# Kernel optimization log

Hardware: AMD Instinct MI355X
Metric: run time of the kernel (lower is better)

## Reference

```python
import jax, jax.numpy as jnp
import numpy as np

N, E, L, F, HID, OUT = 20000, 200000, 5, 4, 128, 3


def _lin(x, w, b):
    # torch Linear convention: w is [out, in]
    return x @ w.T + b


def setup_inputs() -> dict:
    key = jax.random.key(0)
    ks = iter(jax.random.split(key, 40))
    nrm = lambda shape, s=0.05: jax.random.normal(next(ks), shape, dtype=jnp.float32) * s
    inp = {
        'x': jax.random.normal(next(ks), (N, L, F), dtype=jnp.float32),
        'edge_index': jax.random.randint(next(ks), (2, E), 0, N, dtype=jnp.int64),
        'edge_attr': jax.random.normal(next(ks), (E, F), dtype=jnp.float32),
        'batch': jnp.zeros((N,), dtype=jnp.int64),
        'node_type': jax.random.normal(next(ks), (N, 1), dtype=jnp.float32),
        # PastStateEncoder params
        'emb': nrm((L, F), 1.0),
        'conv_w': nrm((HID, 2 * F, 3)),  # Conv1d(8,128,3) OIW
        'conv_b': nrm((HID,)),
        # FusionLayer Linear(129,128)
        'fuse_w': nrm((HID, HID + 1)), 'fuse_b': nrm((HID,)),
        # gnn1 EdgeModel: Linear(2*128+4,128), Linear(128,128)
        'g1e_w1': nrm((HID, 2 * HID + F)), 'g1e_b1': nrm((HID,)),
        'g1e_w2': nrm((HID, HID)), 'g1e_b2': nrm((HID,)),
        # gnn1 NodeModel: Linear(256,128), Linear(128,128)
        'g1n_w1': nrm((HID, 2 * HID)), 'g1n_b1': nrm((HID,)),
        'g1n_w2': nrm((HID, HID)), 'g1n_b2': nrm((HID,)),
        # gnn2 EdgeModel: Linear(2*128+128,128), Linear(128,128)
        'g2e_w1': nrm((HID, 3 * HID)), 'g2e_b1': nrm((HID,)),
        'g2e_w2': nrm((HID, HID)), 'g2e_b2': nrm((HID,)),
        # gnn2 NodeModel
        'g2n_w1': nrm((HID, 2 * HID)), 'g2n_b1': nrm((HID,)),
        'g2n_w2': nrm((HID, HID)), 'g2n_b2': nrm((HID,)),
        # final_mlp: Linear(128,128), BN(128), Linear(128,3)
        'fm_w1': nrm((HID, HID)), 'fm_b1': nrm((HID,)),
        'bn_g': jnp.ones((HID,), dtype=jnp.float32), 'bn_b': jnp.zeros((HID,), dtype=jnp.float32),
        'fm_w2': nrm((OUT, HID)), 'fm_b2': nrm((OUT,)),
    }
    return inp


def _encoder(x, emb, conv_w, conv_b):
    # x: [N, L, F]; append learned positional embedding -> [N, L, 2F]
    n = x.shape[0]
    xe = jnp.concatenate([x, jnp.broadcast_to(emb[None], (n, L, F))], axis=-1)
    xc = xe.transpose(0, 2, 1)  # [N, 2F, L]
    y = jax.lax.conv_general_dilated(
        xc, conv_w, window_strides=(1,), padding=[(1, 1)],
        dimension_numbers=('NCW', 'OIW', 'NCW'))
    y = y + conv_b[None, :, None]
    return y.mean(axis=-1)  # [N, HID]


def _edge_mlp(src, dst, ea, w1, b1, w2, b2):
    h = jax.nn.relu(_lin(jnp.concatenate([src, dst, ea], axis=1), w1, b1))
    return _lin(h, w2, b2)


def _node_mlp(x_row, ea, w1, b1, w2, b2):
    h = jax.nn.relu(_lin(jnp.concatenate([x_row, ea], axis=1), w1, b1))
    return _lin(h, w2, b2)


def reference(x, edge_index, edge_attr, batch, node_type,
              emb, conv_w, conv_b, fuse_w, fuse_b,
              g1e_w1, g1e_b1, g1e_w2, g1e_b2, g1n_w1, g1n_b1, g1n_w2, g1n_b2,
              g2e_w1, g2e_b1, g2e_w2, g2e_b2, g2n_w1, g2n_b1, g2n_w2, g2n_b2,
              fm_w1, fm_b1, bn_g, bn_b, fm_w2, fm_b2):
    row, col = edge_index[0], edge_index[1]
    h = _encoder(x, emb, conv_w, conv_b)                     # [N,128]
    h = _lin(jnp.concatenate([h, node_type], axis=-1), fuse_w, fuse_b)  # [N,128]
    # gnn1 (MetaLayer: edge model then node model; node model here is per-edge)
    ea = _edge_mlp(h[row], h[col], edge_attr, g1e_w1, g1e_b1, g1e_w2, g1e_b2)  # [E,128]
    h = _node_mlp(h[row], ea, g1n_w1, g1n_b1, g1n_w2, g1n_b2)                  # [E,128]
    # gnn2 (h now lives on edges; indices < N <= E remain valid, matching torch)
    ea = _edge_mlp(h[row], h[col], ea, g2e_w1, g2e_b1, g2e_w2, g2e_b2)
    h = _node_mlp(h[row], ea, g2n_w1, g2n_b1, g2n_w2, g2n_b2)
    # final head on edge_attr: Linear -> BatchNorm1d (training stats) -> ReLU -> Linear
    z = _lin(ea, fm_w1, fm_b1)
    mu = z.mean(axis=0)
    var = z.var(axis=0)  # biased, matches torch BN normalization
    z = (z - mu) * jax.lax.rsqrt(var + 1e-5) * bn_g + bn_b
    z = jax.nn.relu(z)
    return _lin(z, fm_w2, fm_b2)  # [E,3]
```

## Files before the change

kernel.cpp:

```cpp
#include <hip/hip_runtime.h>

#define N_NODES 20000
#define N_EDGES 200000
#define HID 128
#define STR 136
#define NBLK 3125
#define NREP 64

typedef unsigned short u16;
using bf16x8 = __attribute__((ext_vector_type(8))) __bf16;
using f32x4  = __attribute__((ext_vector_type(4))) float;

__device__ __forceinline__ u16 f2bf(float f) {
  union { float f; unsigned u; } v; v.f = f;
  unsigned u = v.u;
  return (u16)((u + 0x7FFFu + ((u >> 16) & 1u)) >> 16);
}
__device__ __forceinline__ float bf2f(unsigned s) {
  union { unsigned u; float f; } v; v.u = s << 16;
  return v.f;
}
__device__ __forceinline__ bf16x8 ld8(const u16* p) { return *(const bf16x8*)p; }

__device__ __forceinline__ void zero_acc8(f32x4 acc[4]) {
#pragma unroll
  for (int i = 0; i < 4; ++i) acc[i] = (f32x4){0.f, 0.f, 0.f, 0.f};
}

template <int KSTEPS, typename AF>
__device__ __forceinline__ void wgemm8(const u16* __restrict__ PW, AF afrag,
                                       f32x4 acc[4], int lane, int wave) {
  const u16* pb = PW + (wave * 64 + lane) * 8;
  bf16x8 b[2];
  b[0] = ld8(pb);
#pragma unroll
  for (int ks = 0; ks < KSTEPS; ++ks) {
    const int cur = ks & 1;
    if (ks + 1 < KSTEPS) b[cur ^ 1] = ld8(pb + (ks + 1) * 4096);
#pragma unroll
    for (int mt = 0; mt < 4; ++mt) {
      bf16x8 a = afrag(ks, mt);
      acc[mt] = __builtin_amdgcn_mfma_f32_16x16x32_bf16(a, b[cur], acc[mt], 0, 0, 0);
    }
  }
}

template <bool RELU>
__device__ __forceinline__ void epi_store8(u16* buf, const f32x4 acc[4],
                                           const float* __restrict__ bias,
                                           int lane, int wave) {
  const int c = lane & 15, q = lane >> 4;
  const float bb = bias[wave * 16 + c];
  const int col = wave * 16 + c;
#pragma unroll
  for (int mt = 0; mt < 4; ++mt)
#pragma unroll
    for (int r = 0; r < 4; ++r) {
      float v = acc[mt][r] + bb;
      if (RELU) v = fmaxf(v, 0.f);
      buf[(mt * 16 + q * 4 + r) * STR + col] = f2bf(v);
    }
}

__device__ __forceinline__ void flush_buf8(const u16* buf, u16* __restrict__ gout,
                                           int e0, int tid) {
#pragma unroll
  for (int it = 0; it < 2; ++it) {
    int cid = tid + it * 512, e = cid >> 4, p = cid & 15;
    uint4 v = *(const uint4*)(buf + e * STR + p * 8);
    *(uint4*)(gout + (size_t)(e0 + e) * HID + p * 8) = v;
  }
}

__device__ __forceinline__ void stage_gather8(const int* __restrict__ rowI,
                                              const int* __restrict__ colI,
                                              const u16* __restrict__ htab,
                                              u16* B0, u16* B1,
                                              int e0, int lane, int wave) {
  const int r = lane >> 4, p = lane & 15;
#pragma unroll
  for (int it = 0; it < 4; ++it) {
    int j = wave * 16 + it * 4 + r;
    int e = j & 63;
    int id = (j < 64) ? rowI[e0 + e] : colI[e0 + e];
    uint4 v = *(const uint4*)(htab + (size_t)id * HID + p * 8);
    *(uint4*)(((j < 64) ? B0 : B1) + e * STR + p * 8) = v;
  }
}

__global__ __launch_bounds__(128) void k_prep1(
    const float* __restrict__ emb, const float* __restrict__ conv_w,
    const float* __restrict__ conv_b, const float* __restrict__ fuse_w,
    const float* __restrict__ fuse_b,
    const float* __restrict__ fm_w1, const float* __restrict__ g2e_b2,
    const float* __restrict__ fm_b1, const float* __restrict__ w6,
    float* __restrict__ Mt, float* __restrict__ C0, float* __restrict__ Wnt,
    float* __restrict__ b67, float* __restrict__ W67, float* __restrict__ bnrep) {
  __shared__ float red[22][129];
  __shared__ float w7s[128];
  const int o = blockIdx.x;
  const int j = threadIdx.x;
  bnrep[o * 128 + j] = 0.f;
  float A[21];
  {
    float b0 = conv_b[j];
#pragma unroll
    for (int p = 0; p < 5; ++p) {
#pragma unroll
      for (int i = 0; i < 8; ++i) {
        float s = 0.f;
#pragma unroll
        for (int k = 0; k < 3; ++k) {
          int t = p + 1 - k;
          if (t >= 0 && t < 5) s += conv_w[(j * 8 + i) * 3 + k];
        }
        s *= 0.2f;
        if (i < 4) A[p * 4 + i] = s;
        else b0 += emb[p * 4 + (i - 4)] * s;
      }
    }
    A[20] = b0;
  }
  float w = fuse_w[o * 129 + j];
  float w7 = fm_w1[o * 128 + j];
  w7s[j] = w7;
#pragma unroll
  for (int qq = 0; qq < 21; ++qq) red[qq][j] = w * A[qq];
  red[21][j] = w7 * g2e_b2[j];
  __syncthreads();
  if (j < 22) {
    float s = 0.f;
    for (int t = 0; t < 128; ++t) s += red[j][t];
    if (j < 20)      Mt[j * 128 + o] = s;
    else if (j == 20) C0[o] = s + fuse_b[o];
    else              b67[o] = s + fm_b1[o];
  }
  if (j == 0) Wnt[o] = fuse_w[o * 129 + 128];
  float s = 0.f;
  for (int t = 0; t < 128; ++t) s += w7s[t] * w6[t * 128 + j];
  W67[o * 128 + j] = s;
}

struct PackArgs {
  const float* src[6];
  u16* dst[6];
  int Kin[6];
  int ksCum[7];
};

__global__ __launch_bounds__(256) void k_prep2(
    PackArgs pa, const float* __restrict__ x, const float* __restrict__ node_type,
    const float* __restrict__ Mt, const float* __restrict__ C0,
    const float* __restrict__ Wnt, u16* __restrict__ h2) {
  if (blockIdx.x < 41) {
    int bk = blockIdx.x;
    int mi = 0;
    while (bk >= pa.ksCum[mi + 1]) ++mi;
    int ks = bk - pa.ksCum[mi];
    const float* W = pa.src[mi];
    u16* D = pa.dst[mi] + ks * 4096;
    int Kin = pa.Kin[mi];
#pragma unroll
    for (int t = 0; t < 16; ++t) {
      int el = t * 256 + (int)threadIdx.x;
      int j = el & 7, ln = (el >> 3) & 63, ntile = el >> 9;
      int k = ks * 32 + ((ln >> 4) << 3) + j;
      int n = ntile * 16 + (ln & 15);
      float v = (k < Kin) ? W[n * Kin + k] : 0.0f;
      D[el] = f2bf(v);
    }
    return;
  }
  __shared__ float xs[16][20], nts[16], mts[20 * 128];
  const int tid = threadIdx.x;
  const int n0 = ((int)blockIdx.x - 41) * 16;
  for (int i = tid; i < 320; i += 256) xs[i / 20][i % 20] = x[n0 * 20 + i];
  if (tid < 16) nts[tid] = node_type[n0 + tid];
  for (int i = tid; i < 2560; i += 256) mts[i] = Mt[i];
  __syncthreads();
  const int nl = tid >> 4;
  const int c0 = (tid & 15) * 8;
  float nt = nts[nl];
  union { u16 s[8]; uint4 u; } o;
#pragma unroll
  for (int i = 0; i < 8; ++i) {
    int ch = c0 + i;
    float acc = C0[ch] + Wnt[ch] * nt;
#pragma unroll
    for (int qq = 0; qq < 20; ++qq) acc += xs[nl][qq] * mts[qq * 128 + ch];
    o.s[i] = f2bf(acc);
  }
  *(uint4*)(h2 + (size_t)(n0 + nl) * HID + c0) = o.u;
}

__global__ __launch_bounds__(512, 8) void k_gnn1(
    const int* __restrict__ eidx, const float* __restrict__ eattr,
    const u16* __restrict__ h2, const u16* __restrict__ pW1, const u16* __restrict__ pW2,
    const u16* __restrict__ pW3, const u16* __restrict__ pW4, const float* __restrict__ b1,
    const float* __restrict__ b2, const float* __restrict__ b3, const float* __restrict__ b4,
    u16* __restrict__ ea1, u16* __restrict__ h3) {
  __shared__ __align__(16) u16 B0[64 * STR], B1[64 * STR];
  const int tid = threadIdx.x, lane = tid & 63, wave = tid >> 6;
  const int e0 = blockIdx.x * 64;
  const int m = lane & 15, q = lane >> 4;
  const int aoff = m * STR + q * 8;
  const int* rowI = eidx;
  const int* colI = eidx + N_EDGES;

  stage_gather8(rowI, colI, h2, B0, B1, e0, lane, wave);

  bf16x8 ef[4];
#pragma unroll
  for (int mt = 0; mt < 4; ++mt) {
    union { u16 s[8]; uint4 u; bf16x8 v; } t;
    t.u = make_uint4(0u, 0u, 0u, 0u);
    if (q == 0) {
      float4 a = *(const float4*)(eattr + (size_t)(e0 + mt * 16 + m) * 4);
      t.s[0] = f2bf(a.x); t.s[1] = f2bf(a.y); t.s[2] = f2bf(a.z); t.s[3] = f2bf(a.w);
    }
    ef[mt] = t.v;
  }
  __syncthreads();

  f32x4 acc[4];
  zero_acc8(acc);
  wgemm8<9>(pW1, [&](int ks, int mt) -> bf16x8 {
    if (ks < 4) return ld8(B0 + aoff + mt * 16 * STR + ks * 32);
    if (ks < 8) return ld8(B1 + aoff + mt * 16 * STR + (ks - 4) * 32);
    return ef[mt];
  }, acc, lane, wave);
  __syncthreads();
  epi_store8<true>(B1, acc, b1, lane, wave);
  __syncthreads();

  zero_acc8(acc);
  wgemm8<4>(pW2, [&](int ks, int mt) -> bf16x8 {
    return ld8(B1 + aoff + mt * 16 * STR + ks * 32);
  }, acc, lane, wave);
  epi_store8<false>(B0, acc, b2, lane, wave);
  __syncthreads();
  flush_buf8(B0, ea1, e0, tid);

  if (e0 < N_NODES) {
#pragma unroll
    for (int it = 0; it < 2; ++it) {
      int e = wave * 8 + it * 4 + q;
      int id = rowI[e0 + e];
      uint4 v = *(const uint4*)(h2 + (size_t)id * HID + m * 8);
      *(uint4*)(B1 + e * STR + m * 8) = v;
    }
    __syncthreads();

    zero_acc8(acc);
    wgemm8<8>(pW3, [&](int ks, int mt) -> bf16x8 {
      if (ks < 4) return ld8(B1 + aoff + mt * 16 * STR + ks * 32);
      return ld8(B0 + aoff + mt * 16 * STR + (ks - 4) * 32);
    }, acc, lane, wave);
    __syncthreads();
    epi_store8<true>(B1, acc, b3, lane, wave);
    __syncthreads();

    zero_acc8(acc);
    wgemm8<4>(pW4, [&](int ks, int mt) -> bf16x8 {
      return ld8(B1 + aoff + mt * 16 * STR + ks * 32);
    }, acc, lane, wave);
    epi_store8<false>(B0, acc, b4, lane, wave);
    __syncthreads();
    flush_buf8(B0, h3, e0, tid);
  }
}

__global__ __launch_bounds__(512, 8) void k_gnn2(
    const int* __restrict__ eidx, const u16* __restrict__ h3, u16* ea1z,
    const u16* __restrict__ pW5, const u16* __restrict__ pW67,
    const float* __restrict__ b5, const float* __restrict__ b67,
    float* __restrict__ bnrep) {
  __shared__ __align__(16) u16 B0[64 * STR], B1[64 * STR];
  const int tid = threadIdx.x, lane = tid & 63, wave = tid >> 6;
  const int e0 = blockIdx.x * 64;
  const int m = lane & 15, q = lane >> 4;
  const int aoff = m * STR + q * 8;
  const int* rowI = eidx;
  const int* colI = eidx + N_EDGES;

  stage_gather8(rowI, colI, h3, B0, B1, e0, lane, wave);
  __syncthreads();

  f32x4 acc[4];
  zero_acc8(acc);
  wgemm8<8>(pW5, [&](int ks, int mt) -> bf16x8 {
    if (ks < 4) return ld8(B0 + aoff + mt * 16 * STR + ks * 32);
    return ld8(B1 + aoff + mt * 16 * STR + (ks - 4) * 32);
  }, acc, lane, wave);
  __syncthreads();

#pragma unroll
  for (int it = 0; it < 2; ++it) {
    int cid = tid + it * 512, e = cid >> 4, p = cid & 15;
    uint4 v = *(const uint4*)(ea1z + (size_t)(e0 + e) * HID + p * 8);
    *(uint4*)(B0 + e * STR + p * 8) = v;
  }
  __syncthreads();

  wgemm8<4>(pW5 + 8 * 4096, [&](int ks, int mt) -> bf16x8 {
    return ld8(B0 + aoff + mt * 16 * STR + ks * 32);
  }, acc, lane, wave);
  epi_store8<true>(B1, acc, b5, lane, wave);
  __syncthreads();

  zero_acc8(acc);
  wgemm8<4>(pW67, [&](int ks, int mt) -> bf16x8 {
    return ld8(B1 + aoff + mt * 16 * STR + ks * 32);
  }, acc, lane, wave);

  {
    const int c = lane & 15;
    const int col = wave * 16 + c;
    const float bb = b67[col];
    float s0 = 0.f, q0 = 0.f;
#pragma unroll
    for (int mt = 0; mt < 4; ++mt)
#pragma unroll
      for (int r = 0; r < 4; ++r) {
        float v0 = acc[mt][r] + bb;
        s0 += v0; q0 += v0 * v0;
        int row = mt * 16 + q * 4 + r;
        B0[row * STR + col] = f2bf(v0);
      }
    s0 += __shfl_xor(s0, 16); s0 += __shfl_xor(s0, 32);
    q0 += __shfl_xor(q0, 16); q0 += __shfl_xor(q0, 32);
    if (lane < 16) {
      float* slot = bnrep + ((int)blockIdx.x & (NREP - 1)) * 256;
      atomicAdd(&slot[wave * 16 + lane], s0);
      atomicAdd(&slot[128 + wave * 16 + lane], q0);
    }
  }
  __syncthreads();
  flush_buf8(B0, ea1z, e0, tid);
}

__global__ __launch_bounds__(256) void k_head(const u16* __restrict__ z,
                                              const float* __restrict__ bnrep,
                                              const float* __restrict__ bn_g,
                                              const float* __restrict__ bn_b,
                                              const float* __restrict__ w2,
                                              const float* __restrict__ b2,
                                              float* __restrict__ out) {
  __shared__ float sh_s[128], sh_h[128], sh_w0[128], sh_w1[128], sh_w2[128];
  const int tid = threadIdx.x;
  {
    float s = 0.f;
    for (int r = 0; r < NREP; ++r) s += bnrep[r * 256 + tid];
    __shared__ float acc2[256];
    acc2[tid] = s;
    __syncthreads();
    if (tid < 128) {
      const float inv = 1.0f / (float)N_EDGES;
      float mu = acc2[tid] * inv;
      float var = acc2[128 + tid] * inv - mu * mu;
      float sc = bn_g[tid] * rsqrtf(var + 1e-5f);
      sh_s[tid] = sc;
      sh_h[tid] = bn_b[tid] - mu * sc;
      sh_w0[tid] = w2[tid];
      sh_w1[tid] = w2[128 + tid];
      sh_w2[tid] = w2[256 + tid];
    }
    __syncthreads();
  }
  const int lane = tid & 63, wave = tid >> 6;
  const int g = lane >> 4;
  const int p = lane & 15;
  const int c0 = p * 8;
  const float bb0 = b2[0], bb1 = b2[1], bb2 = b2[2];
#pragma unroll 4
  for (int it = 0; it < 16; ++it) {
    int e = (int)blockIdx.x * 256 + wave * 64 + it * 4 + g;
    if (e >= N_EDGES) break;
    uint4 v = *(const uint4*)(z + (size_t)e * HID + c0);
    unsigned wv[4] = {v.x, v.y, v.z, v.w};
    float a0 = 0.f, a1 = 0.f, a2 = 0.f;
#pragma unroll
    for (int k = 0; k < 4; ++k) {
      int ch = c0 + k * 2;
      float lo = bf2f(wv[k] & 0xffffu), hi = bf2f(wv[k] >> 16);
      float r0 = fmaxf(fmaf(lo, sh_s[ch], sh_h[ch]), 0.f);
      float r1 = fmaxf(fmaf(hi, sh_s[ch + 1], sh_h[ch + 1]), 0.f);
      a0 += r0 * sh_w0[ch] + r1 * sh_w0[ch + 1];
      a1 += r0 * sh_w1[ch] + r1 * sh_w1[ch + 1];
      a2 += r0 * sh_w2[ch] + r1 * sh_w2[ch + 1];
    }
#pragma unroll
    for (int off = 1; off < 16; off <<= 1) {
      a0 += __shfl_xor(a0, off);
      a1 += __shfl_xor(a1, off);
      a2 += __shfl_xor(a2, off);
    }
    if (p < 3) out[e * 3 + p] = (p == 0) ? a0 + bb0 : (p == 1) ? a1 + bb1 : a2 + bb2;
  }
}

extern "C" void kernel_launch(void* const* d_in, const int* in_sizes, int n_in,
                              void* d_out, int out_size, void* d_ws, size_t ws_size,
                              hipStream_t stream) {
  const float* x         = (const float*)d_in[0];
  const int* eidx        = (const int*)d_in[1];
  const float* eattr     = (const float*)d_in[2];
  const float* node_type = (const float*)d_in[4];
  const float* emb       = (const float*)d_in[5];
  const float* conv_w    = (const float*)d_in[6];
  const float* conv_b    = (const float*)d_in[7];
  const float* fuse_w    = (const float*)d_in[8];
  const float* fuse_b    = (const float*)d_in[9];
  const float* g1e_w1    = (const float*)d_in[10];
  const float* g1e_b1    = (const float*)d_in[11];
  const float* g1e_w2    = (const float*)d_in[12];
  const float* g1e_b2    = (const float*)d_in[13];
  const float* g1n_w1    = (const float*)d_in[14];
  const float* g1n_b1    = (const float*)d_in[15];
  const float* g1n_w2    = (const float*)d_in[16];
  const float* g1n_b2    = (const float*)d_in[17];
  const float* g2e_w1    = (const float*)d_in[18];
  const float* g2e_b1    = (const float*)d_in[19];
  const float* g2e_w2    = (const float*)d_in[20];
  const float* g2e_b2    = (const float*)d_in[21];
  const float* fm_w1     = (const float*)d_in[26];
  const float* fm_b1     = (const float*)d_in[27];
  const float* bn_g      = (const float*)d_in[28];
  const float* bn_b      = (const float*)d_in[29];
  const float* fm_w2     = (const float*)d_in[30];
  const float* fm_b2     = (const float*)d_in[31];
  float* out = (float*)d_out;

  char* ws = (char*)d_ws;
  size_t off = 0;
  auto take = [&](size_t bytes) {
    void* p = ws + off;
    off = (off + bytes + 255) & ~(size_t)255;
    return p;
  };
  u16* h2   = (u16*)take((size_t)N_NODES * HID * 2);
  u16* h3   = (u16*)take((size_t)20032 * HID * 2);
  u16* ea1z = (u16*)take((size_t)N_EDGES * HID * 2);
  float* Mt    = (float*)take(20 * 128 * 4);
  float* C0    = (float*)take(128 * 4);
  float* Wnt   = (float*)take(128 * 4);
  float* b67   = (float*)take(128 * 4);
  float* W67f  = (float*)take(128 * 128 * 4);
  float* bnrep = (float*)take((size_t)NREP * 256 * 4);
  u16* pW1  = (u16*)take(9 * 4096 * 2);
  u16* pW2  = (u16*)take(4 * 4096 * 2);
  u16* pW3  = (u16*)take(8 * 4096 * 2);
  u16* pW4  = (u16*)take(4 * 4096 * 2);
  u16* pW5  = (u16*)take(12 * 4096 * 2);
  u16* pW67 = (u16*)take(4 * 4096 * 2);

  k_prep1<<<128, 128, 0, stream>>>(emb, conv_w, conv_b, fuse_w, fuse_b,
                                   fm_w1, g2e_b2, fm_b1, g2e_w2,
                                   Mt, C0, Wnt, b67, W67f, bnrep);

  PackArgs pa;
  const float* srcs[6] = {g1e_w1, g1e_w2, g1n_w1, g1n_w2, g2e_w1, W67f};
  u16* dsts[6] = {pW1, pW2, pW3, pW4, pW5, pW67};
  int kins[6] = {260, 128, 256, 128, 384, 128};
  int kst[6] = {9, 4, 8, 4, 12, 4};
  int cum = 0;
  for (int i = 0; i < 6; ++i) {
    pa.src[i] = srcs[i]; pa.dst[i] = dsts[i]; pa.Kin[i] = kins[i];
    pa.ksCum[i] = cum; cum += kst[i];
  }
  pa.ksCum[6] = cum;

  k_prep2<<<41 + N_NODES / 16, 256, 0, stream>>>(pa, x, node_type, Mt, C0, Wnt, h2);
  k_gnn1<<<NBLK, 512, 0, stream>>>(eidx, eattr, h2, pW1, pW2, pW3, pW4,
                                   g1e_b1, g1e_b2, g1n_b1, g1n_b2, ea1z, h3);
  k_gnn2<<<NBLK, 512, 0, stream>>>(eidx, h3, ea1z, pW5, pW67,
                                   g2e_b1, b67, bnrep);
  k_head<<<(N_EDGES + 255) / 256, 256, 0, stream>>>(ea1z, bnrep, bn_g, bn_b,
                                                    fm_w2, fm_b2, out);
}
```

Measured before the change: 232.4 us.

## Switch GNN GEMMs to 32x32x16 MFMA tiles with two split accumulators

Replaces the 16x16x32 MFMA scheme, where each wave owned a 16-column strip across four row tiles, with 32x32x16 MFMA. Waves now tile the 64x128 output as 2 row tiles by 4 column tiles. Alternating K-steps go into two separate accumulators to break the MFMA dependency chain, and the packed-weight layout, epilogue and BN-stat reduction are rewritten to match. Each wave now loads fewer weight fragments per output. In exchange it needs more accumulator registers, and the occupancy hint drops from 8 to 6.

```diff
diff --git a/kernel.cpp b/kernel.cpp
--- a/kernel.cpp
+++ b/kernel.cpp
@@ -10,6 +10,7 @@
 typedef unsigned short u16;
 using bf16x8 = __attribute__((ext_vector_type(8))) __bf16;
 using f32x4  = __attribute__((ext_vector_type(4))) float;
+using f32x16 = __attribute__((ext_vector_type(16))) float;
 
 __device__ __forceinline__ u16 f2bf(float f) {
   union { float f; unsigned u; } v; v.f = f;
@@ -22,44 +23,44 @@
 }
 __device__ __forceinline__ bf16x8 ld8(const u16* p) { return *(const bf16x8*)p; }
 
-__device__ __forceinline__ void zero_acc8(f32x4 acc[4]) {
-#pragma unroll
-  for (int i = 0; i < 4; ++i) acc[i] = (f32x4){0.f, 0.f, 0.f, 0.f};
-}
-
-template <int KSTEPS, typename AF>
-__device__ __forceinline__ void wgemm8(const u16* __restrict__ PW, AF afrag,
-                                       f32x4 acc[4], int lane, int wave) {
-  const u16* pb = PW + (wave * 64 + lane) * 8;
+__device__ __forceinline__ f32x16 zf16() {
+  f32x16 z = {0.f,0.f,0.f,0.f,0.f,0.f,0.f,0.f,0.f,0.f,0.f,0.f,0.f,0.f,0.f,0.f};
+  return z;
+}
+
+template <int KS16, typename AF>
+__device__ __forceinline__ void wgemm32(const u16* __restrict__ PW, AF afrag,
+                                        f32x16& accA, f32x16& accB,
+                                        int lane, int ct) {
+  const u16* pb = PW + ct * 512 + lane * 8;
   bf16x8 b[2];
   b[0] = ld8(pb);
 #pragma unroll
-  for (int ks = 0; ks < KSTEPS; ++ks) {
-    const int cur = ks & 1;
-    if (ks + 1 < KSTEPS) b[cur ^ 1] = ld8(pb + (ks + 1) * 4096);
-#pragma unroll
-    for (int mt = 0; mt < 4; ++mt) {
-      bf16x8 a = afrag(ks, mt);
-      acc[mt] = __builtin_amdgcn_mfma_f32_16x16x32_bf16(a, b[cur], acc[mt], 0, 0, 0);
-    }
+  for (int s = 0; s < KS16; ++s) {
+    const int cur = s & 1;
+    if (s + 1 < KS16) b[cur ^ 1] = ld8(pb + (s + 1) * 2048);
+    bf16x8 a = afrag(s);
+    if (cur == 0)
+      accA = __builtin_amdgcn_mfma_f32_32x32x16_bf16(a, b[cur], accA, 0, 0, 0);
+    else
+      accB = __builtin_amdgcn_mfma_f32_32x32x16_bf16(a, b[cur], accB, 0, 0, 0);
   }
 }
 
 template <bool RELU>
-__device__ __forceinline__ void epi_store8(u16* buf, const f32x4 acc[4],
-                                           const float* __restrict__ bias,
-                                           int lane, int wave) {
-  const int c = lane & 15, q = lane >> 4;
-  const float bb = bias[wave * 16 + c];
-  const int col = wave * 16 + c;
-#pragma unroll
-  for (int mt = 0; mt < 4; ++mt)
-#pragma unroll
-    for (int r = 0; r < 4; ++r) {
-      float v = acc[mt][r] + bb;
-      if (RELU) v = fmaxf(v, 0.f);
-      buf[(mt * 16 + q * 4 + r) * STR + col] = f2bf(v);
-    }
+__device__ __forceinline__ void epi_store32(u16* buf, f32x16 acc,
+                                            const float* __restrict__ bias,
+                                            int lane, int rt, int ct) {
+  const int col = ct * 32 + (lane & 31);
+  const int hi = lane >> 5;
+  const float bb = bias[col];
+#pragma unroll
+  for (int reg = 0; reg < 16; ++reg) {
+    int row = rt * 32 + (reg & 3) + 8 * (reg >> 2) + 4 * hi;
+    float v = acc[reg] + bb;
+    if (RELU) v = fmaxf(v, 0.f);
+    buf[row * STR + col] = f2bf(v);
+  }
 }
 
 __device__ __forceinline__ void flush_buf8(const u16* buf, u16* __restrict__ gout,
@@ -163,9 +164,9 @@
 #pragma unroll
     for (int t = 0; t < 16; ++t) {
       int el = t * 256 + (int)threadIdx.x;
-      int j = el & 7, ln = (el >> 3) & 63, ntile = el >> 9;
-      int k = ks * 32 + ((ln >> 4) << 3) + j;
-      int n = ntile * 16 + (ln & 15);
+      int j = el & 7, l = (el >> 3) & 63, ct = (el >> 9) & 3, s2 = el >> 11;
+      int k = ks * 32 + s2 * 16 + ((l >> 5) << 3) + j;
+      int n = ct * 32 + (l & 31);
       float v = (k < Kin) ? W[n * Kin + k] : 0.0f;
       D[el] = f2bf(v);
     }
@@ -193,7 +194,7 @@
   *(uint4*)(h2 + (size_t)(n0 + nl) * HID + c0) = o.u;
 }
 
-__global__ __launch_bounds__(512, 8) void k_gnn1(
+__global__ __launch_bounds__(512, 6) void k_gnn1(
     const int* __restrict__ eidx, const float* __restrict__ eattr,
     const u16* __restrict__ h2, const u16* __restrict__ pW1, const u16* __restrict__ pW2,
     const u16* __restrict__ pW3, const u16* __restrict__ pW4, const float* __restrict__ b1,
@@ -202,75 +203,73 @@
   __shared__ __align__(16) u16 B0[64 * STR], B1[64 * STR];
   const int tid = threadIdx.x, lane = tid & 63, wave = tid >> 6;
   const int e0 = blockIdx.x * 64;
-  const int m = lane & 15, q = lane >> 4;
-  const int aoff = m * STR + q * 8;
+  const int rt = wave & 1, ct = wave >> 1;
+  const int aoff = (rt * 32 + (lane & 31)) * STR + ((lane >> 5) << 3);
   const int* rowI = eidx;
   const int* colI = eidx + N_EDGES;
 
   stage_gather8(rowI, colI, h2, B0, B1, e0, lane, wave);
 
-  bf16x8 ef[4];
-#pragma unroll
-  for (int mt = 0; mt < 4; ++mt) {
+  bf16x8 ef;
+  {
     union { u16 s[8]; uint4 u; bf16x8 v; } t;
     t.u = make_uint4(0u, 0u, 0u, 0u);
-    if (q == 0) {
-      float4 a = *(const float4*)(eattr + (size_t)(e0 + mt * 16 + m) * 4);
+    if (lane < 32) {
+      float4 a = *(const float4*)(eattr + (size_t)(e0 + rt * 32 + (lane & 31)) * 4);
       t.s[0] = f2bf(a.x); t.s[1] = f2bf(a.y); t.s[2] = f2bf(a.z); t.s[3] = f2bf(a.w);
     }
-    ef[mt] = t.v;
-  }
-  __syncthreads();
-
-  f32x4 acc[4];
-  zero_acc8(acc);
-  wgemm8<9>(pW1, [&](int ks, int mt) -> bf16x8 {
-    if (ks < 4) return ld8(B0 + aoff + mt * 16 * STR + ks * 32);
-    if (ks < 8) return ld8(B1 + aoff + mt * 16 * STR + (ks - 4) * 32);
-    return ef[mt];
-  }, acc, lane, wave);
-  __syncthreads();
-  epi_store8<true>(B1, acc, b1, lane, wave);
-  __syncthreads();
-
-  zero_acc8(acc);
-  wgemm8<4>(pW2, [&](int ks, int mt) -> bf16x8 {
-    return ld8(B1 + aoff + mt * 16 * STR + ks * 32);
-  }, acc, lane, wave);
-  epi_store8<false>(B0, acc, b2, lane, wave);
+    ef = t.v;
+  }
+  __syncthreads();
+
+  f32x16 accA = zf16(), accB = zf16();
+  wgemm32<17>(pW1, [&](int s) -> bf16x8 {
+    if (s < 8) return ld8(B0 + aoff + s * 16);
+    if (s < 16) return ld8(B1 + aoff + (s - 8) * 16);
+    return ef;
+  }, accA, accB, lane, ct);
+  __syncthreads();
+  epi_store32<true>(B1, accA + accB, b1, lane, rt, ct);
+  __syncthreads();
+
+  accA = zf16(); accB = zf16();
+  wgemm32<8>(pW2, [&](int s) -> bf16x8 {
+    return ld8(B1 + aoff + s * 16);
+  }, accA, accB, lane, ct);
+  epi_store32<false>(B0, accA + accB, b2, lane, rt, ct);
   __syncthreads();
   flush_buf8(B0, ea1, e0, tid);
 
   if (e0 < N_NODES) {
 #pragma unroll
     for (int it = 0; it < 2; ++it) {
-      int e = wave * 8 + it * 4 + q;
+      int cid = tid + it * 512, e = cid >> 4, p = cid & 15;
       int id = rowI[e0 + e];
-      uint4 v = *(const uint4*)(h2 + (size_t)id * HID + m * 8);
-      *(uint4*)(B1 + e * STR + m * 8) = v;
-    }
-    __syncthreads();
-
-    zero_acc8(acc);
-    wgemm8<8>(pW3, [&](int ks, int mt) -> bf16x8 {
-      if (ks < 4) return ld8(B1 + aoff + mt * 16 * STR + ks * 32);
-      return ld8(B0 + aoff + mt * 16 * STR + (ks - 4) * 32);
-    }, acc, lane, wave);
-    __syncthreads();
-    epi_store8<true>(B1, acc, b3, lane, wave);
-    __syncthreads();
-
-    zero_acc8(acc);
-    wgemm8<4>(pW4, [&](int ks, int mt) -> bf16x8 {
-      return ld8(B1 + aoff + mt * 16 * STR + ks * 32);
-    }, acc, lane, wave);
-    epi_store8<false>(B0, acc, b4, lane, wave);
+      uint4 v = *(const uint4*)(h2 + (size_t)id * HID + p * 8);
+      *(uint4*)(B1 + e * STR + p * 8) = v;
+    }
+    __syncthreads();
+
+    accA = zf16(); accB = zf16();
+    wgemm32<16>(pW3, [&](int s) -> bf16x8 {
+      if (s < 8) return ld8(B1 + aoff + s * 16);
+      return ld8(B0 + aoff + (s - 8) * 16);
+    }, accA, accB, lane, ct);
+    __syncthreads();
+    epi_store32<true>(B1, accA + accB, b3, lane, rt, ct);
+    __syncthreads();
+
+    accA = zf16(); accB = zf16();
+    wgemm32<8>(pW4, [&](int s) -> bf16x8 {
+      return ld8(B1 + aoff + s * 16);
+    }, accA, accB, lane, ct);
+    epi_store32<false>(B0, accA + accB, b4, lane, rt, ct);
     __syncthreads();
     flush_buf8(B0, h3, e0, tid);
   }
 }
 
-__global__ __launch_bounds__(512, 8) void k_gnn2(
+__global__ __launch_bounds__(512, 6) void k_gnn2(
     const int* __restrict__ eidx, const u16* __restrict__ h3, u16* ea1z,
     const u16* __restrict__ pW5, const u16* __restrict__ pW67,
     const float* __restrict__ b5, const float* __restrict__ b67,
@@ -278,20 +277,19 @@
   __shared__ __align__(16) u16 B0[64 * STR], B1[64 * STR];
   const int tid = threadIdx.x, lane = tid & 63, wave = tid >> 6;
   const int e0 = blockIdx.x * 64;
-  const int m = lane & 15, q = lane >> 4;
-  const int aoff = m * STR + q * 8;
+  const int rt = wave & 1, ct = wave >> 1;
+  const int aoff = (rt * 32 + (lane & 31)) * STR + ((lane >> 5) << 3);
   const int* rowI = eidx;
   const int* colI = eidx + N_EDGES;
 
   stage_gather8(rowI, colI, h3, B0, B1, e0, lane, wave);
   __syncthreads();
 
-  f32x4 acc[4];
-  zero_acc8(acc);
-  wgemm8<8>(pW5, [&](int ks, int mt) -> bf16x8 {
-    if (ks < 4) return ld8(B0 + aoff + mt * 16 * STR + ks * 32);
-    return ld8(B1 + aoff + mt * 16 * STR + (ks - 4) * 32);
-  }, acc, lane, wave);
+  f32x16 accA = zf16(), accB = zf16();
+  wgemm32<16>(pW5, [&](int s) -> bf16x8 {
+    if (s < 8) return ld8(B0 + aoff + s * 16);
+    return ld8(B1 + aoff + (s - 8) * 16);
+  }, accA, accB, lane, ct);
   __syncthreads();
 
 #pragma unroll
@@ -302,37 +300,36 @@
   }
   __syncthreads();
 
-  wgemm8<4>(pW5 + 8 * 4096, [&](int ks, int mt) -> bf16x8 {
-    return ld8(B0 + aoff + mt * 16 * STR + ks * 32);
-  }, acc, lane, wave);
-  epi_store8<true>(B1, acc, b5, lane, wave);
-  __syncthreads();
-
-  zero_acc8(acc);
-  wgemm8<4>(pW67, [&](int ks, int mt) -> bf16x8 {
-    return ld8(B1 + aoff + mt * 16 * STR + ks * 32);
-  }, acc, lane, wave);
+  wgemm32<8>(pW5 + 16 * 2048, [&](int s) -> bf16x8 {
+    return ld8(B0 + aoff + s * 16);
+  }, accA, accB, lane, ct);
+  epi_store32<true>(B1, accA + accB, b5, lane, rt, ct);
+  __syncthreads();
+
+  accA = zf16(); accB = zf16();
+  wgemm32<8>(pW67, [&](int s) -> bf16x8 {
+    return ld8(B1 + aoff + s * 16);
+  }, accA, accB, lane, ct);
 
   {
-    const int c = lane & 15;
-    const int col = wave * 16 + c;
+    f32x16 acc = accA + accB;
+    const int col = ct * 32 + (lane & 31);
+    const int hi = lane >> 5;
     const float bb = b67[col];
     float s0 = 0.f, q0 = 0.f;
 #pragma unroll
-    for (int mt = 0; mt < 4; ++mt)
-#pragma unroll
-      for (int r = 0; r < 4; ++r) {
-        float v0 = acc[mt][r] + bb;
-        s0 += v0; q0 += v0 * v0;
-        int row = mt * 16 + q * 4 + r;
-        B0[row * STR + col] = f2bf(v0);
-      }
-    s0 += __shfl_xor(s0, 16); s0 += __shfl_xor(s0, 32);
-    q0 += __shfl_xor(q0, 16); q0 += __shfl_xor(q0, 32);
-    if (lane < 16) {
+    for (int reg = 0; reg < 16; ++reg) {
+      float v = acc[reg] + bb;
+      s0 += v; q0 += v * v;
+      int row = rt * 32 + (reg & 3) + 8 * (reg >> 2) + 4 * hi;
+      B0[row * STR + col] = f2bf(v);
+    }
+    s0 += __shfl_xor(s0, 32);
+    q0 += __shfl_xor(q0, 32);
+    if (lane < 32) {
       float* slot = bnrep + ((int)blockIdx.x & (NREP - 1)) * 256;
-      atomicAdd(&slot[wave * 16 + lane], s0);
-      atomicAdd(&slot[128 + wave * 16 + lane], q0);
+      atomicAdd(&slot[col], s0);
+      atomicAdd(&slot[128 + col], q0);
     }
   }
   __syncthreads();
```

Result: no change. 236.1 us (+1.6%).

## Preload weight fragments into registers ahead of gathers and barriers

Applied to the files above, without the earlier changes.

Replaces the double-buffered weight-fragment loop with bulk register preloads of all K-step B fragments. Each preload is issued early, before the gather, barrier or epilogue it precedes, so global weight latency overlaps other work. This raises register pressure, so launch bounds are relaxed from 8 to 4 blocks per CU, which lowers occupancy. The gnn1 row re-gather is also remapped so consecutive threads read contiguous 16-byte chunks of each row, giving coalesced loads.

```diff
diff --git a/kernel.cpp b/kernel.cpp
--- a/kernel.cpp
+++ b/kernel.cpp
@@ -27,22 +27,22 @@
   for (int i = 0; i < 4; ++i) acc[i] = (f32x4){0.f, 0.f, 0.f, 0.f};
 }
 
-template <int KSTEPS, typename AF>
-__device__ __forceinline__ void wgemm8(const u16* __restrict__ PW, AF afrag,
-                                       f32x4 acc[4], int lane, int wave) {
+template <int K>
+__device__ __forceinline__ void load_b(bf16x8 (&b)[K], const u16* __restrict__ PW,
+                                       int lane, int wave) {
   const u16* pb = PW + (wave * 64 + lane) * 8;
-  bf16x8 b[2];
-  b[0] = ld8(pb);
-#pragma unroll
-  for (int ks = 0; ks < KSTEPS; ++ks) {
-    const int cur = ks & 1;
-    if (ks + 1 < KSTEPS) b[cur ^ 1] = ld8(pb + (ks + 1) * 4096);
-#pragma unroll
-    for (int mt = 0; mt < 4; ++mt) {
-      bf16x8 a = afrag(ks, mt);
-      acc[mt] = __builtin_amdgcn_mfma_f32_16x16x32_bf16(a, b[cur], acc[mt], 0, 0, 0);
-    }
-  }
+#pragma unroll
+  for (int s = 0; s < K; ++s) b[s] = ld8(pb + s * 4096);
+}
+
+template <int K, typename AF>
+__device__ __forceinline__ void mfma_steps(const bf16x8 (&b)[K], AF afrag,
+                                           f32x4 acc[4]) {
+#pragma unroll
+  for (int s = 0; s < K; ++s)
+#pragma unroll
+    for (int mt = 0; mt < 4; ++mt)
+      acc[mt] = __builtin_amdgcn_mfma_f32_16x16x32_bf16(afrag(s, mt), b[s], acc[mt], 0, 0, 0);
 }
 
 template <bool RELU>
@@ -193,7 +193,7 @@
   *(uint4*)(h2 + (size_t)(n0 + nl) * HID + c0) = o.u;
 }
 
-__global__ __launch_bounds__(512, 8) void k_gnn1(
+__global__ __launch_bounds__(512, 4) void k_gnn1(
     const int* __restrict__ eidx, const float* __restrict__ eattr,
     const u16* __restrict__ h2, const u16* __restrict__ pW1, const u16* __restrict__ pW2,
     const u16* __restrict__ pW3, const u16* __restrict__ pW4, const float* __restrict__ b1,
@@ -207,6 +207,9 @@
   const int* rowI = eidx;
   const int* colI = eidx + N_EDGES;
 
+  bf16x8 b1r[9];
+  load_b(b1r, pW1, lane, wave);
+
   stage_gather8(rowI, colI, h2, B0, B1, e0, lane, wave);
 
   bf16x8 ef[4];
@@ -224,53 +227,59 @@
 
   f32x4 acc[4];
   zero_acc8(acc);
-  wgemm8<9>(pW1, [&](int ks, int mt) -> bf16x8 {
+  mfma_steps<9>(b1r, [&](int ks, int mt) -> bf16x8 {
     if (ks < 4) return ld8(B0 + aoff + mt * 16 * STR + ks * 32);
     if (ks < 8) return ld8(B1 + aoff + mt * 16 * STR + (ks - 4) * 32);
     return ef[mt];
-  }, acc, lane, wave);
+  }, acc);
+  bf16x8 b2r[4];
+  load_b(b2r, pW2, lane, wave);
   __syncthreads();
   epi_store8<true>(B1, acc, b1, lane, wave);
   __syncthreads();
 
   zero_acc8(acc);
-  wgemm8<4>(pW2, [&](int ks, int mt) -> bf16x8 {
+  mfma_steps<4>(b2r, [&](int ks, int mt) -> bf16x8 {
     return ld8(B1 + aoff + mt * 16 * STR + ks * 32);
-  }, acc, lane, wave);
+  }, acc);
   epi_store8<false>(B0, acc, b2, lane, wave);
   __syncthreads();
   flush_buf8(B0, ea1, e0, tid);
 
   if (e0 < N_NODES) {
+    bf16x8 b3r[8];
+    load_b(b3r, pW3, lane, wave);
 #pragma unroll
     for (int it = 0; it < 2; ++it) {
-      int e = wave * 8 + it * 4 + q;
+      int cid = tid + it * 512, e = cid >> 4, p = cid & 15;
       int id = rowI[e0 + e];
-      uint4 v = *(const uint4*)(h2 + (size_t)id * HID + m * 8);
-      *(uint4*)(B1 + e * STR + m * 8) = v;
+      uint4 v = *(const uint4*)(h2 + (size_t)id * HID + p * 8);
+      *(uint4*)(B1 + e * STR + p * 8) = v;
     }
     __syncthreads();
 
     zero_acc8(acc);
-    wgemm8<8>(pW3, [&](int ks, int mt) -> bf16x8 {
+    mfma_steps<8>(b3r, [&](int ks, int mt) -> bf16x8 {
       if (ks < 4) return ld8(B1 + aoff + mt * 16 * STR + ks * 32);
       return ld8(B0 + aoff + mt * 16 * STR + (ks - 4) * 32);
-    }, acc, lane, wave);
+    }, acc);
+    bf16x8 b4r[4];
+    load_b(b4r, pW4, lane, wave);
     __syncthreads();
     epi_store8<true>(B1, acc, b3, lane, wave);
     __syncthreads();
 
     zero_acc8(acc);
-    wgemm8<4>(pW4, [&](int ks, int mt) -> bf16x8 {
+    mfma_steps<4>(b4r, [&](int ks, int mt) -> bf16x8 {
       return ld8(B1 + aoff + mt * 16 * STR + ks * 32);
-    }, acc, lane, wave);
+    }, acc);
     epi_store8<false>(B0, acc, b4, lane, wave);
     __syncthreads();
     flush_buf8(B0, h3, e0, tid);
   }
 }
 
-__global__ __launch_bounds__(512, 8) void k_gnn2(
+__global__ __launch_bounds__(512, 4) void k_gnn2(
     const int* __restrict__ eidx, const u16* __restrict__ h3, u16* ea1z,
     const u16* __restrict__ pW5, const u16* __restrict__ pW67,
     const float* __restrict__ b5, const float* __restrict__ b67,
@@ -283,15 +292,20 @@
   const int* rowI = eidx;
   const int* colI = eidx + N_EDGES;
 
+  bf16x8 bar[8];
+  load_b(bar, pW5, lane, wave);
+
   stage_gather8(rowI, colI, h3, B0, B1, e0, lane, wave);
   __syncthreads();
 
   f32x4 acc[4];
   zero_acc8(acc);
-  wgemm8<8>(pW5, [&](int ks, int mt) -> bf16x8 {
+  bf16x8 bbr[4];
+  load_b(bbr, pW5 + 8 * 4096, lane, wave);
+  mfma_steps<8>(bar, [&](int ks, int mt) -> bf16x8 {
     if (ks < 4) return ld8(B0 + aoff + mt * 16 * STR + ks * 32);
     return ld8(B1 + aoff + mt * 16 * STR + (ks - 4) * 32);
-  }, acc, lane, wave);
+  }, acc);
   __syncthreads();
 
 #pragma unroll
@@ -300,18 +314,20 @@
     uint4 v = *(const uint4*)(ea1z + (size_t)(e0 + e) * HID + p * 8);
     *(uint4*)(B0 + e * STR + p * 8) = v;
   }
-  __syncthreads();
-
-  wgemm8<4>(pW5 + 8 * 4096, [&](int ks, int mt) -> bf16x8 {
+  bf16x8 bcr[4];
+  load_b(bcr, pW67, lane, wave);
+  __syncthreads();
+
+  mfma_steps<4>(bbr, [&](int ks, int mt) -> bf16x8 {
     return ld8(B0 + aoff + mt * 16 * STR + ks * 32);
-  }, acc, lane, wave);
+  }, acc);
   epi_store8<true>(B1, acc, b5, lane, wave);
   __syncthreads();
 
   zero_acc8(acc);
-  wgemm8<4>(pW67, [&](int ks, int mt) -> bf16x8 {
+  mfma_steps<4>(bcr, [&](int ks, int mt) -> bf16x8 {
     return ld8(B1 + aoff + mt * 16 * STR + ks * 32);
-  }, acc, lane, wave);
+  }, acc);
 
   {
     const int c = lane & 15;
```

Result: slower. 246.8 us (+6.2%).
